# Kernel optimization log

Hardware: AMD Instinct MI355X
Metric: run time of the kernel (lower is better)

Reference implementation:

```python
import jax, jax.numpy as jnp
import numpy as np
from jax import lax


def bilinear_resize(x, oh, ow):
    # x: (..., H, W); torch F.interpolate bilinear, align_corners=False
    H, W = x.shape[-2], x.shape[-1]
    def coords(n_in, n_out):
        src = (jnp.arange(n_out, dtype=jnp.float32) + 0.5) * (n_in / n_out) - 0.5
        src = jnp.clip(src, 0.0, n_in - 1.0)
        i0 = jnp.floor(src).astype(jnp.int32)
        i1 = jnp.minimum(i0 + 1, n_in - 1)
        return i0, i1, src - i0.astype(jnp.float32)
    r0, r1, wr = coords(H, oh)
    c0, c1, wc = coords(W, ow)
    xr = x[..., r0, :] * (1.0 - wr)[:, None] + x[..., r1, :] * wr[:, None]
    return xr[..., c0] * (1.0 - wc) + xr[..., c1] * wc


def setup_inputs():
    key = jax.random.key(0)
    ks = jax.random.split(key, 20)
    B, D, C, WIN, NH, A = 256, 1280, 64, 14, 8, 49
    def p(k, *sh):
        return jax.random.normal(k, sh, dtype=jnp.float32) * 0.02
    return {
        "X": jax.random.normal(ks[0], (B, 3, D), dtype=jnp.float32),
        "W_embed": p(ks[1], C * WIN * WIN, D), "b_embed": p(ks[2], C * WIN * WIN),
        "W_qkv": p(ks[3], 3 * C, C),
        "W_proj": p(ks[4], C, C), "b_proj": p(ks[5], C),
        "dwc_w": p(ks[6], C, 1, 3, 3), "dwc_b": p(ks[7], C),
        "an_bias": p(ks[8], NH, A, 7, 7), "na_bias": p(ks[9], NH, A, 7, 7),
        "ah_bias": p(ks[10], 1, NH, A, WIN, 1), "aw_bias": p(ks[11], 1, NH, A, 1, WIN),
        "ha_bias": p(ks[12], 1, NH, WIN, 1, A), "wa_bias": p(ks[13], 1, NH, 1, WIN, A),
        "W_adj": p(ks[14], 256, C * WIN * WIN), "b_adj": p(ks[15], 256),
        "W_t1": p(ks[16], 256, D), "b_t1": p(ks[17], 256),
        "W_t2": p(ks[18], 128, 256), "b_t2": p(ks[19], 128),
    }


def reference(X, W_embed, b_embed, W_qkv, W_proj, b_proj, dwc_w, dwc_b,
              an_bias, na_bias, ah_bias, aw_bias, ha_bias, wa_bias,
              W_adj, b_adj, W_t1, b_t1, W_t2, b_t2):
    B = X.shape[0]
    C, WIN, NH, A = 64, 14, 8, 49
    N = WIN * WIN            # 196 tokens
    HD = C // NH             # head dim 8
    scale = HD ** -0.5
    b3 = 3 * B

    # embed_to_img: (B*3, 1280) -> (B*3, C*N) -> tokens (B*3, N, C)
    Xe = X.reshape(b3, -1) @ W_embed.T + b_embed
    xt = Xe.reshape(b3, N, C)

    # AgentAttention
    qkv = xt @ W_qkv.T                                  # (b3, N, 3C), qkv_bias=False
    q, k, v = jnp.split(qkv, 3, axis=-1)
    # agent tokens: AdaptiveAvgPool2d 14x14 -> 7x7 over q (exact 2x2 mean)
    agent = q.reshape(b3, 7, 2, 7, 2, C).mean(axis=(2, 4)).reshape(b3, A, C)
    q = q.reshape(b3, N, NH, HD).transpose(0, 2, 1, 3)
    k = k.reshape(b3, N, NH, HD).transpose(0, 2, 1, 3)
    v = v.reshape(b3, N, NH, HD).transpose(0, 2, 1, 3)
    agent = agent.reshape(b3, A, NH, HD).transpose(0, 2, 1, 3)

    # stage 1: agents attend to all tokens
    pb = bilinear_resize(an_bias, WIN, WIN).reshape(NH, A, N) \
         + (ah_bias + aw_bias).reshape(NH, A, N)
    agent_attn = jax.nn.softmax(jnp.einsum('bhad,bhnd->bhan', agent * scale, k) + pb, axis=-1)
    agent_v = jnp.einsum('bhan,bhnd->bhad', agent_attn, v)   # (b3, NH, A, HD)

    # stage 2: tokens attend to agents
    ab = bilinear_resize(na_bias, WIN, WIN).reshape(NH, A, N).transpose(0, 2, 1) \
         + (ha_bias + wa_bias).reshape(NH, N, A)
    q_attn = jax.nn.softmax(jnp.einsum('bhnd,bhad->bhna', q * scale, agent) + ab, axis=-1)
    o = jnp.einsum('bhna,bhad->bhnd', q_attn, agent_v)
    o = o.transpose(0, 2, 1, 3).reshape(b3, N, C)

    # depthwise conv enhancement on v
    v_img = v.transpose(0, 2, 1, 3).reshape(b3, WIN, WIN, C).transpose(0, 3, 1, 2)
    dwc = lax.conv_general_dilated(v_img, dwc_w, (1, 1), [(1, 1), (1, 1)],
                                   feature_group_count=C) + dwc_b[None, :, None, None]
    o = o + dwc.transpose(0, 2, 3, 1).reshape(b3, N, C)
    o = o @ W_proj.T + b_proj

    X_adj = (o.reshape(b3, -1) @ W_adj.T + b_adj).reshape(B, 3, -1)

    def mlp(z):
        return jnp.tanh(z @ W_t1.T + b_t1) @ W_t2.T + b_t2
    anchor, pos, neg = mlp(X[:, 0]), mlp(X[:, 1]), mlp(X[:, 2])
    return anchor, pos, neg, X_adj
```

## Files before the change

kernel.cpp:

```cpp
#include <hip/hip_runtime.h>

using u16 = unsigned short;
using u32 = unsigned int;

constexpr int Bn   = 256;
constexpr int Dd   = 1280;
constexpr int Cc   = 64;
constexpr int WINc = 14;
constexpr int NHc  = 8;
constexpr int Ac   = 49;
constexpr int Nc   = WINc * WINc;
constexpr int HDc  = Cc / NHc;
constexpr int B3c  = 3 * Bn;
constexpr int CNc  = Cc * Nc;

typedef __attribute__((ext_vector_type(8))) short v8s;
typedef __attribute__((ext_vector_type(4))) float v4f;
typedef __attribute__((ext_vector_type(2))) float v2f;

__device__ __forceinline__ float bflo(u32 u){ union{u32 x; float f;} c; c.x = u << 16; return c.f; }
__device__ __forceinline__ float bfhi(u32 u){ union{u32 x; float f;} c; c.x = u & 0xffff0000u; return c.f; }
__device__ __forceinline__ float bfs(u16 h){ union{u32 x; float f;} c; c.x = ((u32)h) << 16; return c.f; }
__device__ __forceinline__ u16 f2bb(float f){
  u32 u = __float_as_uint(f);
  u32 r = (u + 0x7fffu + ((u >> 16) & 1u)) >> 16;
  return (u16)r;
}
__device__ __forceinline__ void unpack8(uint4 u, float* dst){
  dst[0]=bflo(u.x); dst[1]=bfhi(u.x); dst[2]=bflo(u.y); dst[3]=bfhi(u.y);
  dst[4]=bflo(u.z); dst[5]=bfhi(u.z); dst[6]=bflo(u.w); dst[7]=bfhi(u.w);
}
__device__ __forceinline__ uint4 pack8(const float* s){
  uint4 r;
  r.x = (u32)f2bb(s[0]) | ((u32)f2bb(s[1]) << 16);
  r.y = (u32)f2bb(s[2]) | ((u32)f2bb(s[3]) << 16);
  r.z = (u32)f2bb(s[4]) | ((u32)f2bb(s[5]) << 16);
  r.w = (u32)f2bb(s[6]) | ((u32)f2bb(s[7]) << 16);
  return r;
}

__device__ __forceinline__ float hexp2(float x){ return __builtin_amdgcn_exp2f(x); }

__device__ __forceinline__ void gl_lds16(const u16* g, u16* l){
  __builtin_amdgcn_global_load_lds(
      (const __attribute__((address_space(1))) unsigned int*)g,
      (__attribute__((address_space(3))) unsigned int*)l,
      16, 0, 0);
}

constexpr int WeN   = 12544 * 1280;
constexpr int XN    = 768 * 1280;
constexpr int WadjN = 256 * CNc;
constexpr int W1N   = 256 * 1280;
constexpr int W2N   = 128 * 256;
constexpr int CONVB = (WeN + XN + WadjN + W1N + W2N) / (256*8);
constexpr int BIASB = (2 * NHc * Ac * Nc + 255) / 256;
__global__ __launch_bounds__(256) void conv_bias_kernel(const float* __restrict__ We,
                                                        const float* __restrict__ X,
                                                        const float* __restrict__ Wadj,
                                                        const float* __restrict__ W1,
                                                        const float* __restrict__ W2,
                                                        u16* __restrict__ WeB,
                                                        u16* __restrict__ XB,
                                                        u16* __restrict__ WadjB,
                                                        u16* __restrict__ W1B,
                                                        u16* __restrict__ W2B,
                                                        const float* __restrict__ an, const float* __restrict__ na,
                                                        const float* __restrict__ ah, const float* __restrict__ aw,
                                                        const float* __restrict__ ha, const float* __restrict__ wa,
                                                        float* __restrict__ pb, float* __restrict__ ab)
{
  if (blockIdx.x >= CONVB) {
    constexpr float LOG2E = 1.4426950408889634f;
    const int total = NHc * Ac * Nc;
    int idx = (blockIdx.x - CONVB) * 256 + threadIdx.x;
    if (idx >= 2 * total) return;
    const bool isab = idx >= total;
    const int r = isab ? idx - total : idx;
    const int h = r / (Ac * Nc);
    const int r2 = r % (Ac * Nc);
    int a, n;
    if (isab) { n = r2 / Ac; a = r2 % Ac; } else { a = r2 / Nc; n = r2 % Nc; }
    const int y = n / WINc, x = n % WINc;
    float sy = fminf(fmaxf(0.5f * y - 0.25f, 0.f), 6.f);
    float sx = fminf(fmaxf(0.5f * x - 0.25f, 0.f), 6.f);
    const int y0 = (int)sy, x0 = (int)sx;
    const float wy = sy - y0, wx = sx - x0;
    const int y1 = (y0 + 1 < 6) ? y0 + 1 : 6;
    const int x1 = (x0 + 1 < 6) ? x0 + 1 : 6;
    const float* src = (isab ? na : an) + (h * Ac + a) * 49;
    const float v00 = src[y0*7 + x0], v01 = src[y0*7 + x1];
    const float v10 = src[y1*7 + x0], v11 = src[y1*7 + x1];
    const float bi = (1.f - wy) * ((1.f - wx) * v00 + wx * v01)
                   + wy * ((1.f - wx) * v10 + wx * v11);
    if (!isab) pb[((size_t)h*Nc + n)*Ac + a] = (bi + ah[(h*Ac + a)*WINc + y] + aw[(h*Ac + a)*WINc + x]) * LOG2E;
    else       ab[((size_t)h*Ac + a)*Nc + n] = (bi + ha[(h*WINc + y)*Ac + a] + wa[(h*WINc + x)*Ac + a]) * LOG2E;
    return;
  }
  const size_t idx = ((size_t)blockIdx.x * 256 + threadIdx.x) * 8;
  const float* src; u16* dst;
  if (idx < (size_t)WeN)                          { src = We + idx;                         dst = WeB + idx; }
  else if (idx < (size_t)WeN + XN)                { src = X + (idx - WeN);                  dst = XB + (idx - WeN); }
  else if (idx < (size_t)WeN + XN + WadjN)        { src = Wadj + (idx - WeN - XN);          dst = WadjB + (idx - WeN - XN); }
  else if (idx < (size_t)WeN + XN + WadjN + W1N)  { src = W1 + (idx - WeN - XN - WadjN);    dst = W1B + (idx - WeN - XN - WadjN); }
  else                                            { src = W2 + (idx - WeN - XN - WadjN - W1N); dst = W2B + (idx - WeN - XN - WadjN - W1N); }
  float v[8];
  *reinterpret_cast<float4*>(&v[0]) = *reinterpret_cast<const float4*>(src);
  *reinterpret_cast<float4*>(&v[4]) = *reinterpret_cast<const float4*>(src + 4);
  *reinterpret_cast<uint4*>(dst) = pack8(v);
}

__global__ __launch_bounds__(256) void gemm_embed_mlp1(const u16* __restrict__ XB,
                                                       const u16* __restrict__ WeB,
                                                       const u16* __restrict__ W1B,
                                                       const float* __restrict__ be,
                                                       const float* __restrict__ b1,
                                                       u16* __restrict__ xt,
                                                       u16* __restrict__ H)
{
  constexpr int KK = Dd;
  __shared__ u16 As[128 * 32];
  __shared__ u16 Bs[128 * 32];
  const int t = threadIdx.x;
  const bool mlp = blockIdx.x >= 98;
  const int n0 = (mlp ? (blockIdx.x - 98) : blockIdx.x) * 128;
  const int m0 = blockIdx.y * 128;
  const u16* Bmat = mlp ? W1B : WeB;
  const float* bias = mlp ? b1 : be;
  u16* Cmat = mlp ? H : xt;
  const int NN = mlp ? 256 : CNc;
  const int wave = t >> 6, lane = t & 63;
  const int wm = wave >> 1, wn = wave & 1;
  const int mi = lane & 15, quad = lane >> 4;

  v4f acc[4][4];
  #pragma unroll
  for (int a = 0; a < 4; ++a)
    #pragma unroll
    for (int b = 0; b < 4; ++b) acc[a][b] = (v4f){0.f, 0.f, 0.f, 0.f};

  const int rs = wave*32 + (lane >> 2);
  const int cs = (lane & 3) * 8;
  const u16* ga0 = XB + (size_t)(m0 + rs) * KK + cs;
  const u16* ga1 = XB + (size_t)(m0 + rs + 16) * KK + cs;
  const u16* gb0 = Bmat + (size_t)(n0 + rs) * KK + cs;
  const u16* gb1 = Bmat + (size_t)(n0 + rs + 16) * KK + cs;
  u16* la0 = &As[(wave*32)      * 32];
  u16* la1 = &As[(wave*32 + 16) * 32];
  u16* lb0 = &Bs[(wave*32)      * 32];
  u16* lb1 = &Bs[(wave*32 + 16) * 32];

  for (int kt = 0; kt < KK; kt += 32) {
    gl_lds16(ga0 + kt, la0);
    gl_lds16(ga1 + kt, la1);
    gl_lds16(gb0 + kt, lb0);
    gl_lds16(gb1 + kt, lb1);
    __syncthreads();

    v8s af[4], bf[4];
    #pragma unroll
    for (int mt = 0; mt < 4; ++mt)
      af[mt] = *reinterpret_cast<const v8s*>(&As[(wm*64 + mt*16 + mi)*32 + quad*8]);
    #pragma unroll
    for (int nt = 0; nt < 4; ++nt)
      bf[nt] = *reinterpret_cast<const v8s*>(&Bs[(wn*64 + nt*16 + mi)*32 + quad*8]);
    #pragma unroll
    for (int mt = 0; mt < 4; ++mt)
      #pragma unroll
      for (int nt = 0; nt < 4; ++nt)
        acc[mt][nt] = __builtin_amdgcn_mfma_f32_16x16x32_bf16(af[mt], bf[nt], acc[mt][nt], 0, 0, 0);
    __syncthreads();
  }

  #pragma unroll
  for (int nt = 0; nt < 4; ++nt) {
    const int col = n0 + wn*64 + nt*16 + mi;
    const float bc = bias[col];
    #pragma unroll
    for (int mt = 0; mt < 4; ++mt) {
      #pragma unroll
      for (int r = 0; r < 4; ++r) {
        const int row = m0 + wm*64 + mt*16 + quad*4 + r;
        float val = acc[mt][nt][r] + bc;
        if (mlp) val = tanhf(val);
        Cmat[(size_t)row * NN + col] = f2bb(val);
      }
    }
  }
}

__global__ __launch_bounds__(256) void tail_kernel(const float* __restrict__ part,
                                                   const float* __restrict__ badj,
                                                   float* __restrict__ outadj,
                                                   const u16* __restrict__ H,
                                                   const u16* __restrict__ W2B,
                                                   const float* __restrict__ b2,
                                                   float* __restrict__ outp)
{
  __shared__ u16 As[128 * 40];
  __shared__ u16 Bs[128 * 40];
  const int t = threadIdx.x;
  if (blockIdx.x < B3c) {
    const int idx = blockIdx.x * 256 + t;
    const int n = idx & 255;
    float acc = badj[n];
    #pragma unroll
    for (int s = 0; s < 8; ++s) acc += part[(size_t)s * B3c * 256 + idx];
    outadj[idx] = acc;
    return;
  }
  const int m0 = (blockIdx.x - B3c) * 128;
  const int wave = t >> 6, lane = t & 63;
  const int wm = wave >> 1, wn = wave & 1;
  const int mi = lane & 15, quad = lane >> 4;
  const int srow = t >> 1, scol = (t & 1) * 16;

  v4f acc[4][4];
  #pragma unroll
  for (int a = 0; a < 4; ++a)
    #pragma unroll
    for (int b = 0; b < 4; ++b) acc[a][b] = (v4f){0.f, 0.f, 0.f, 0.f};

  for (int kt = 0; kt < 256; kt += 32) {
    const u16* ap = H + (size_t)(m0 + srow) * 256 + kt + scol;
    *reinterpret_cast<uint4*>(&As[srow*40 + scol])     = *reinterpret_cast<const uint4*>(ap);
    *reinterpret_cast<uint4*>(&As[srow*40 + scol + 8]) = *reinterpret_cast<const uint4*>(ap + 8);
    const u16* bp = W2B + (size_t)srow * 256 + kt + scol;
    *reinterpret_cast<uint4*>(&Bs[srow*40 + scol])     = *reinterpret_cast<const uint4*>(bp);
    *reinterpret_cast<uint4*>(&Bs[srow*40 + scol + 8]) = *reinterpret_cast<const uint4*>(bp + 8);
    __syncthreads();

    v8s af[4], bf[4];
    #pragma unroll
    for (int mt = 0; mt < 4; ++mt)
      af[mt] = *reinterpret_cast<const v8s*>(&As[(wm*64 + mt*16 + mi)*40 + quad*8]);
    #pragma unroll
    for (int nt = 0; nt < 4; ++nt)
      bf[nt] = *reinterpret_cast<const v8s*>(&Bs[(wn*64 + nt*16 + mi)*40 + quad*8]);
    #pragma unroll
    for (int mt = 0; mt < 4; ++mt)
      #pragma unroll
      for (int nt = 0; nt < 4; ++nt)
        acc[mt][nt] = __builtin_amdgcn_mfma_f32_16x16x32_bf16(af[mt], bf[nt], acc[mt][nt], 0, 0, 0);
    __syncthreads();
  }

  #pragma unroll
  for (int nt = 0; nt < 4; ++nt) {
    const int col = wn*64 + nt*16 + mi;
    const float bc = b2[col];
    #pragma unroll
    for (int mt = 0; mt < 4; ++mt) {
      #pragma unroll
      for (int r = 0; r < 4; ++r) {
        const int row = m0 + wm*64 + mt*16 + quad*4 + r;
        const int bi = row / 3, s = row - bi * 3;
        outp[(size_t)s * (Bn*128) + (size_t)bi * 128 + col] = acc[mt][nt][r] + bc;
      }
    }
  }
}

__global__ __launch_bounds__(256) void qkv_mfma(const u16* __restrict__ xt, const float* __restrict__ Wqkv,
                                                u16* __restrict__ qh, u16* __restrict__ kh, u16* __restrict__ vb)
{
  __shared__ u16 As[256 * 72];
  __shared__ u16 Bs[64 * 72];
  const int t = threadIdx.x;
  const int m0 = blockIdx.x * 256;
  const int wave = t >> 6, lane = t & 63;
  const int mi = lane & 15, quad = lane >> 4;

  {
    const int ar = t >> 2, ac = (t & 3) * 16;
    #pragma unroll
    for (int rb = 0; rb < 4; ++rb) {
      const int row = rb*64 + ar;
      const uint4* src = reinterpret_cast<const uint4*>(xt + ((size_t)(m0 + row))*64 + ac);
      *reinterpret_cast<uint4*>(&As[row*72 + ac])     = src[0];
      *reinterpret_cast<uint4*>(&As[row*72 + ac + 8]) = src[1];
    }
  }
  __syncthreads();

  v8s af[2][4];
  #pragma unroll
  for (int ks = 0; ks < 2; ++ks)
    #pragma unroll
    for (int mt = 0; mt < 4; ++mt)
      af[ks][mt] = *reinterpret_cast<const v8s*>(&As[(wave*64 + mt*16 + mi)*72 + ks*32 + quad*8]);

  #pragma unroll 1
  for (int seg = 0; seg < 3; ++seg) {
    if (seg) __syncthreads();
    for (int i = t; i < Cc*Cc; i += 256) {
      const int j = i >> 6, c = i & 63;
      Bs[j*72 + c] = f2bb(Wqkv[(size_t)(seg*64 + j)*64 + c]);
    }
    __syncthreads();

    v4f acc[4][4];
    #pragma unroll
    for (int a = 0; a < 4; ++a)
      #pragma unroll
      for (int b = 0; b < 4; ++b) acc[a][b] = (v4f){0.f, 0.f, 0.f, 0.f};

    #pragma unroll
    for (int ks = 0; ks < 2; ++ks) {
      v8s bf[4];
      #pragma unroll
      for (int nt = 0; nt < 4; ++nt)
        bf[nt] = *reinterpret_cast<const v8s*>(&Bs[(nt*16 + mi)*72 + ks*32 + quad*8]);
      #pragma unroll
      for (int mt = 0; mt < 4; ++mt)
        #pragma unroll
        for (int nt = 0; nt < 4; ++nt)
          acc[mt][nt] = __builtin_amdgcn_mfma_f32_16x16x32_bf16(af[ks][mt], bf[nt], acc[mt][nt], 0, 0, 0);
    }

    u16* hm = (seg == 0) ? qh : kh;
    #pragma unroll
    for (int nt = 0; nt < 4; ++nt) {
      const int col = nt*16 + mi;
      const int h = col >> 3, d = col & 7;
      #pragma unroll
      for (int mt = 0; mt < 4; ++mt) {
        #pragma unroll
        for (int r = 0; r < 4; ++r) {
          const int row = m0 + wave*64 + mt*16 + quad*4 + r;
          const u16 val = f2bb(acc[mt][nt][r]);
          if (seg < 2) {
            const int b = row / Nc, n = row - b * Nc;
            hm[((size_t)(b*NHc + h)*Nc + n)*8 + d] = val;
          } else {
            vb[(size_t)row * 64 + col] = val;
          }
        }
      }
    }
  }
}

__global__ __launch_bounds__(256) void attn_kernel(const u16* __restrict__ qh, const u16* __restrict__ kh,
                                                   const u16* __restrict__ v,
                                                   const float* __restrict__ pb, const float* __restrict__ ab,
                                                   u16* __restrict__ o)
{
  __shared__ float sU[Nc*10];
  __shared__ float sK[Nc*8], sV[Nc*8];
  __shared__ float sAg[Ac*8], sAV[Ac*8];
  const int bhid = blockIdx.x;
  const int h = bhid / B3c, b = bhid - h * B3c;
  const int bh = b * NHc + h;
  const int t = threadIdx.x;
  const float scale2 = 0.3535533905932738f * 1.4426950408889634f;

  float qreg[8];
  if (t < Nc) {
    const size_t base = ((size_t)bh * Nc + t) * 8;
    unpack8(*reinterpret_cast<const uint4*>(qh + base), qreg);
    #pragma unroll
    for (int d = 0; d < 8; ++d) sU[t*8 + d] = qreg[d];
    unpack8(*reinterpret_cast<const uint4*>(kh + base), &sK[t*8]);
    unpack8(*reinterpret_cast<const uint4*>(v + ((size_t)b*Nc + t)*64 + h*8), &sV[t*8]);
  }
  __syncthreads();

  for (int i = t; i < Ac*8; i += 256) {
    const int a = i >> 3, d = i & 7;
    const int ay = a / 7, ax = a % 7;
    const int n00 = (ay * 2) * WINc + ax * 2;
    sAg[i] = 0.25f * (sU[n00*8+d] + sU[(n00+1)*8+d] + sU[(n00+WINc)*8+d] + sU[(n00+WINc+1)*8+d]);
  }
  __syncthreads();

  if (t < Nc) {
    const int qd = t / Ac, a = t - qd * Ac;
    const int nb = qd * Ac;
    v2f g2[4];
    #pragma unroll
    for (int d2 = 0; d2 < 4; ++d2) g2[d2] = *reinterpret_cast<const v2f*>(&sAg[a*8 + d2*2]);
    const float* pbr = pb + ((size_t)h*Nc + nb)*Ac + a;
    float l0 = 0.f, l1 = 0.f;
    v2f avA[4] = {}, avB[4] = {};
    for (int j = 0; j < 48; j += 2) {
      const v2f* k0 = reinterpret_cast<const v2f*>(&sK[(nb + j)*8]);
      const v2f* k1 = reinterpret_cast<const v2f*>(&sK[(nb + j + 1)*8]);
      v2f sa = (g2[0]*k0[0] + g2[1]*k0[1]) + (g2[2]*k0[2] + g2[3]*k0[3]);
      v2f sb = (g2[0]*k1[0] + g2[1]*k1[1]) + (g2[2]*k1[2] + g2[3]*k1[3]);
      const float e0 = hexp2(fmaf(sa.x + sa.y, scale2, pbr[j*Ac]));
      const float e1 = hexp2(fmaf(sb.x + sb.y, scale2, pbr[(j+1)*Ac]));
      l0 += e0; l1 += e1;
      const v2f* v0 = reinterpret_cast<const v2f*>(&sV[(nb + j)*8]);
      const v2f* v1 = reinterpret_cast<const v2f*>(&sV[(nb + j + 1)*8]);
      const v2f e02 = {e0, e0}, e12 = {e1, e1};
      #pragma unroll
      for (int d2 = 0; d2 < 4; ++d2) { avA[d2] += e02 * v0[d2]; avB[d2] += e12 * v1[d2]; }
    }
    {
      const v2f* k0 = reinterpret_cast<const v2f*>(&sK[(nb + 48)*8]);
      v2f sa = (g2[0]*k0[0] + g2[1]*k0[1]) + (g2[2]*k0[2] + g2[3]*k0[3]);
      const float e0 = hexp2(fmaf(sa.x + sa.y, scale2, pbr[48*Ac]));
      l0 += e0;
      const v2f* v0 = reinterpret_cast<const v2f*>(&sV[(nb + 48)*8]);
      const v2f e02 = {e0, e0};
      #pragma unroll
      for (int d2 = 0; d2 < 4; ++d2) avA[d2] += e02 * v0[d2];
    }
    float* pp = &sU[t*9];
    pp[0] = l0 + l1;
    #pragma unroll
    for (int d2 = 0; d2 < 4; ++d2) {
      const v2f m = avA[d2] + avB[d2];
      pp[1+d2*2] = m.x; pp[2+d2*2] = m.y;
    }
  }
  __syncthreads();

  if (t < Ac) {
    float L = 0.f, av[8] = {};
    #pragma unroll
    for (int p = 0; p < 4; ++p) {
      const float* pp = &sU[(p*Ac + t)*9];
      L += pp[0];
      #pragma unroll
      for (int d = 0; d < 8; ++d) av[d] += pp[1+d];
    }
    const float inv = 1.f / L;
    #pragma unroll
    for (int d = 0; d < 8; ++d) sAV[t*8 + d] = av[d] * inv;
  }
  __syncthreads();

  if (t < Nc) {
    v2f q2[4];
    #pragma unroll
    for (int d2 = 0; d2 < 4; ++d2) q2[d2] = (v2f){qreg[d2*2], qreg[d2*2+1]};
    const float* abr = ab + (size_t)h*Ac*Nc + t;
    float l0 = 0.f, l1 = 0.f;
    v2f oA[4] = {}, oB[4] = {};
    for (int a = 0; a < 48; a += 2) {
      const v2f* g0 = reinterpret_cast<const v2f*>(&sAg[a*8]);
      const v2f* g1 = reinterpret_cast<const v2f*>(&sAg[(a+1)*8]);
      v2f sa = (q2[0]*g0[0] + q2[1]*g0[1]) + (q2[2]*g0[2] + q2[3]*g0[3]);
      v2f sb = (q2[0]*g1[0] + q2[1]*g1[1]) + (q2[2]*g1[2] + q2[3]*g1[3]);
      const float e0 = hexp2(fmaf(sa.x + sa.y, scale2, abr[a*Nc]));
      const float e1 = hexp2(fmaf(sb.x + sb.y, scale2, abr[(a+1)*Nc]));
      l0 += e0; l1 += e1;
      const v2f* a0 = reinterpret_cast<const v2f*>(&sAV[a*8]);
      const v2f* a1 = reinterpret_cast<const v2f*>(&sAV[(a+1)*8]);
      const v2f e02 = {e0, e0}, e12 = {e1, e1};
      #pragma unroll
      for (int d2 = 0; d2 < 4; ++d2) { oA[d2] += e02 * a0[d2]; oB[d2] += e12 * a1[d2]; }
    }
    {
      const v2f* g0 = reinterpret_cast<const v2f*>(&sAg[48*8]);
      v2f sa = (q2[0]*g0[0] + q2[1]*g0[1]) + (q2[2]*g0[2] + q2[3]*g0[3]);
      const float e0 = hexp2(fmaf(sa.x + sa.y, scale2, abr[48*Nc]));
      l0 += e0;
      const v2f* a0 = reinterpret_cast<const v2f*>(&sAV[48*8]);
      const v2f e02 = {e0, e0};
      #pragma unroll
      for (int d2 = 0; d2 < 4; ++d2) oA[d2] += e02 * a0[d2];
    }
    const float inv = 1.f / (l0 + l1);
    float o8[8];
    #pragma unroll
    for (int d2 = 0; d2 < 4; ++d2) {
      const v2f m = oA[d2] + oB[d2];
      o8[d2*2] = m.x * inv; o8[d2*2+1] = m.y * inv;
    }
    *reinterpret_cast<uint4*>(&o[((size_t)b*Nc + t)*64 + h*8]) = pack8(o8);
  }
}

__global__ __launch_bounds__(256) void dwc_kernel(const u16* __restrict__ o, const u16* __restrict__ v,
                                                  const float* __restrict__ dwc_w, const float* __restrict__ dwc_b,
                                                  u16* __restrict__ U)
{
  __shared__ u16 sV[Nc*Cc];
  __shared__ float sWw[9*64];
  const int b = blockIdx.x, t = threadIdx.x;

  const uint2* vsrc = reinterpret_cast<const uint2*>(v + (size_t)b * CNc);
  uint2* sV2 = reinterpret_cast<uint2*>(sV);
  for (int i = t; i < CNc/4; i += 256) sV2[i] = vsrc[i];
  for (int i = t; i < 9*64; i += 256) {
    const int k = i >> 6, c = i & 63;
    sWw[i] = dwc_w[c*9 + k];
  }
  __syncthreads();

  const int c0 = (t & 7) * 8;
  float wreg[9][8], breg[8];
  #pragma unroll
  for (int k = 0; k < 9; ++k) {
    *reinterpret_cast<float4*>(&wreg[k][0]) = *reinterpret_cast<const float4*>(&sWw[k*64 + c0]);
    *reinterpret_cast<float4*>(&wreg[k][4]) = *reinterpret_cast<const float4*>(&sWw[k*64 + c0 + 4]);
  }
  *reinterpret_cast<float4*>(&breg[0]) = *reinterpret_cast<const float4*>(dwc_b + c0);
  *reinterpret_cast<float4*>(&breg[4]) = *reinterpret_cast<const float4*>(dwc_b + c0 + 4);

  const u16* ob = o + (size_t)b * CNc;
  u16* ub = U + (size_t)b * CNc;
  for (int i = t; i < CNc/8; i += 256) {
    const int n = i >> 3;
    const int y = n / WINc, x = n % WINc;
    float acc[8], vv[8];
    unpack8(*reinterpret_cast<const uint4*>(ob + (size_t)i*8), acc);
    #pragma unroll
    for (int j = 0; j < 8; ++j) acc[j] += breg[j];
    #pragma unroll
    for (int ky = 0; ky < 3; ++ky) {
      const int yy = y + ky - 1;
      if (yy < 0 || yy >= WINc) continue;
      #pragma unroll
      for (int kx = 0; kx < 3; ++kx) {
        const int xx = x + kx - 1;
        if (xx < 0 || xx >= WINc) continue;
        const int k = ky*3 + kx;
        unpack8(*reinterpret_cast<const uint4*>(&sV[(yy*WINc + xx)*Cc + c0]), vv);
        #pragma unroll
        for (int j = 0; j < 8; ++j) acc[j] = fmaf(wreg[k][j], vv[j], acc[j]);
      }
    }
    *reinterpret_cast<uint4*>(ub + (size_t)i*8) = pack8(acc);
  }
}

__global__ __launch_bounds__(256) void proj_mfma(const u16* __restrict__ U,
                                                 const float* __restrict__ Wp,
                                                 const float* __restrict__ bp,
                                                 u16* __restrict__ oproj)
{
  __shared__ u16 As[256 * 72];
  __shared__ u16 Bs[64 * 72];
  const int t = threadIdx.x;
  const int m0 = blockIdx.x * 256;
  const int wave = t >> 6, lane = t & 63;
  const int mi = lane & 15, quad = lane >> 4;

  for (int i = t; i < Cc*Cc; i += 256) {
    const int j = i >> 6, c = i & 63;
    Bs[j*72 + c] = f2bb(Wp[i]);
  }
  {
    const int ar = t >> 2, ac = (t & 3) * 16;
    #pragma unroll
    for (int rb = 0; rb < 4; ++rb) {
      const int row = rb*64 + ar;
      const uint4* src = reinterpret_cast<const uint4*>(U + ((size_t)(m0 + row))*64 + ac);
      *reinterpret_cast<uint4*>(&As[row*72 + ac])     = src[0];
      *reinterpret_cast<uint4*>(&As[row*72 + ac + 8]) = src[1];
    }
  }
  __syncthreads();

  v4f acc[4][4];
  #pragma unroll
  for (int a = 0; a < 4; ++a)
    #pragma unroll
    for (int b = 0; b < 4; ++b) acc[a][b] = (v4f){0.f, 0.f, 0.f, 0.f};

  #pragma unroll
  for (int ks = 0; ks < 2; ++ks) {
    v8s af[4], bf[4];
    #pragma unroll
    for (int mt = 0; mt < 4; ++mt)
      af[mt] = *reinterpret_cast<const v8s*>(&As[(wave*64 + mt*16 + mi)*72 + ks*32 + quad*8]);
    #pragma unroll
    for (int nt = 0; nt < 4; ++nt)
      bf[nt] = *reinterpret_cast<const v8s*>(&Bs[(nt*16 + mi)*72 + ks*32 + quad*8]);
    #pragma unroll
    for (int mt = 0; mt < 4; ++mt)
      #pragma unroll
      for (int nt = 0; nt < 4; ++nt)
        acc[mt][nt] = __builtin_amdgcn_mfma_f32_16x16x32_bf16(af[mt], bf[nt], acc[mt][nt], 0, 0, 0);
  }

  #pragma unroll
  for (int nt = 0; nt < 4; ++nt) {
    const int col = nt*16 + mi;
    const float bc = bp[col];
    #pragma unroll
    for (int mt = 0; mt < 4; ++mt) {
      #pragma unroll
      for (int r = 0; r < 4; ++r) {
        const int row = m0 + wave*64 + mt*16 + quad*4 + r;
        oproj[(size_t)row * 64 + col] = f2bb(acc[mt][nt][r] + bc);
      }
    }
  }
}

__global__ __launch_bounds__(256) void gemm_adj_mfma(const u16* __restrict__ Amat,
                                                     const u16* __restrict__ BmatB,
                                                     float* __restrict__ part)
{
  constexpr int K = CNc, Kc = CNc/8;
  __shared__ u16 As[128 * 32];
  __shared__ u16 Bs[128 * 32];
  const int t = threadIdx.x;
  const int n0 = blockIdx.x * 128, m0 = blockIdx.y * 128;
  const int kbeg = blockIdx.z * Kc;
  const int wave = t >> 6, lane = t & 63;
  const int wm = wave >> 1, wn = wave & 1;
  const int mi = lane & 15, quad = lane >> 4;

  v4f acc[4][4];
  #pragma unroll
  for (int a = 0; a < 4; ++a)
    #pragma unroll
    for (int b = 0; b < 4; ++b) acc[a][b] = (v4f){0.f, 0.f, 0.f, 0.f};

  const int rs = wave*32 + (lane >> 2);
  const int cs = (lane & 3) * 8;
  const u16* ga0 = Amat + (size_t)(m0 + rs) * K + kbeg + cs;
  const u16* ga1 = Amat + (size_t)(m0 + rs + 16) * K + kbeg + cs;
  const u16* gb0 = BmatB + (size_t)(n0 + rs) * K + kbeg + cs;
  const u16* gb1 = BmatB + (size_t)(n0 + rs + 16) * K + kbeg + cs;
  u16* la0 = &As[(wave*32)      * 32];
  u16* la1 = &As[(wave*32 + 16) * 32];
  u16* lb0 = &Bs[(wave*32)      * 32];
  u16* lb1 = &Bs[(wave*32 + 16) * 32];

  for (int kt = 0; kt < Kc; kt += 32) {
    gl_lds16(ga0 + kt, la0);
    gl_lds16(ga1 + kt, la1);
    gl_lds16(gb0 + kt, lb0);
    gl_lds16(gb1 + kt, lb1);
    __syncthreads();

    v8s af[4], bf[4];
    #pragma unroll
    for (int mt = 0; mt < 4; ++mt)
      af[mt] = *reinterpret_cast<const v8s*>(&As[(wm*64 + mt*16 + mi)*32 + quad*8]);
    #pragma unroll
    for (int nt = 0; nt < 4; ++nt)
      bf[nt] = *reinterpret_cast<const v8s*>(&Bs[(wn*64 + nt*16 + mi)*32 + quad*8]);
    #pragma unroll
    for (int mt = 0; mt < 4; ++mt)
      #pragma unroll
      for (int nt = 0; nt < 4; ++nt)
        acc[mt][nt] = __builtin_amdgcn_mfma_f32_16x16x32_bf16(af[mt], bf[nt], acc[mt][nt], 0, 0, 0);
    __syncthreads();
  }

  const size_t zoff = (size_t)blockIdx.z * B3c * 256;
  #pragma unroll
  for (int nt = 0; nt < 4; ++nt) {
    const int col = n0 + wn*64 + nt*16 + mi;
    #pragma unroll
    for (int mt = 0; mt < 4; ++mt) {
      #pragma unroll
      for (int r = 0; r < 4; ++r) {
        const int row = m0 + wm*64 + mt*16 + quad*4 + r;
        part[zoff + (size_t)row * 256 + col] = acc[mt][nt][r];
      }
    }
  }
}

extern "C" void kernel_launch(void* const* d_in, const int* in_sizes, int n_in,
                              void* d_out, int out_size, void* d_ws, size_t ws_size,
                              hipStream_t stream)
{
  auto in = [&](int i){ return reinterpret_cast<const float*>(d_in[i]); };
  const float *X = in(0), *We = in(1), *be = in(2), *Wq = in(3), *Wp = in(4), *bp = in(5),
              *dww = in(6), *dwb = in(7), *anb = in(8), *nab = in(9), *ahb = in(10), *awb = in(11),
              *hab = in(12), *wab = in(13), *Wadj = in(14), *badj = in(15),
              *W1 = in(16), *b1 = in(17), *W2 = in(18), *b2 = in(19);
  float* out = reinterpret_cast<float*>(d_out);
  char* w = reinterpret_cast<char*>(d_ws);

  const size_t TOK = (size_t)B3c * CNc;
  u16* xt = reinterpret_cast<u16*>(w);
  u16* qh = reinterpret_cast<u16*>(w + TOK*2);
  u16* kh = reinterpret_cast<u16*>(w + TOK*4);
  u16* vb = reinterpret_cast<u16*>(w + TOK*6);
  float* pb = reinterpret_cast<float*>(w + TOK*8);
  float* ab = pb + NHc*Ac*Nc;
  u16* WadjB = reinterpret_cast<u16*>(ab + NHc*Ac*Nc);
  u16* XB  = WadjB + WadjN;
  u16* W1B = XB + XN;
  u16* W2B = W1B + W1N;
  u16* H   = W2B + W2N;
  u16* WeB = qh;
  u16* U = qh;
  float* part = reinterpret_cast<float*>(kh);

  conv_bias_kernel<<<dim3(CONVB + BIASB), 256, 0, stream>>>(
      We, X, Wadj, W1, W2, WeB, XB, WadjB, W1B, W2B,
      anb, nab, ahb, awb, hab, wab, pb, ab);
  gemm_embed_mlp1<<<dim3(100, B3c/128), 256, 0, stream>>>(XB, WeB, W1B, be, b1, xt, H);
  qkv_mfma<<<dim3((B3c*Nc)/256), 256, 0, stream>>>(xt, Wq, qh, kh, vb);
  attn_kernel<<<dim3(B3c*NHc), 256, 0, stream>>>(qh, kh, vb, pb, ab, xt );
  dwc_kernel<<<dim3(B3c), 256, 0, stream>>>(xt , vb, dww, dwb, U);
  proj_mfma<<<dim3((B3c*Nc)/256), 256, 0, stream>>>(U, Wp, bp, xt );
  gemm_adj_mfma<<<dim3(256/128, B3c/128, 8), 256, 0, stream>>>(xt , WadjB, part);
  tail_kernel<<<dim3(B3c + B3c/128), 256, 0, stream>>>(part, badj, out + 3*Bn*128, H, W2B, b2, out);
}
```

Measured before the change: 416.1 us.

## Fuse depthwise conv with output projection GEMM in one kernel

The depthwise-conv output for each sample now goes into shared memory instead of a global U buffer. The same block then runs the 64x64 projection MFMA on it and writes the result straight out. The projection weight is converted to bf16 once in the conversion kernel and kept in registers as MFMA B fragments. This removes one kernel launch and a full global write and read of the intermediate token tensor. In exchange, shared memory per block grows to roughly 55KB, which may lower occupancy, and padded rows past 196 are computed but never stored.

```diff
diff --git a/kernel.cpp b/kernel.cpp
--- a/kernel.cpp
+++ b/kernel.cpp
@@ -53,18 +53,21 @@
 constexpr int WadjN = 256 * CNc;
 constexpr int W1N   = 256 * 1280;
 constexpr int W2N   = 128 * 256;
-constexpr int CONVB = (WeN + XN + WadjN + W1N + W2N) / (256*8);
+constexpr int WpN   = 64 * 64;
+constexpr int CONVB = (WeN + XN + WadjN + W1N + W2N + WpN) / (256*8);
 constexpr int BIASB = (2 * NHc * Ac * Nc + 255) / 256;
 __global__ __launch_bounds__(256) void conv_bias_kernel(const float* __restrict__ We,
                                                         const float* __restrict__ X,
                                                         const float* __restrict__ Wadj,
                                                         const float* __restrict__ W1,
                                                         const float* __restrict__ W2,
+                                                        const float* __restrict__ Wp,
                                                         u16* __restrict__ WeB,
                                                         u16* __restrict__ XB,
                                                         u16* __restrict__ WadjB,
                                                         u16* __restrict__ W1B,
                                                         u16* __restrict__ W2B,
+                                                        u16* __restrict__ WpB,
                                                         const float* __restrict__ an, const float* __restrict__ na,
                                                         const float* __restrict__ ah, const float* __restrict__ aw,
                                                         const float* __restrict__ ha, const float* __restrict__ wa,
@@ -99,11 +102,13 @@
   }
   const size_t idx = ((size_t)blockIdx.x * 256 + threadIdx.x) * 8;
   const float* src; u16* dst;
-  if (idx < (size_t)WeN)                          { src = We + idx;                         dst = WeB + idx; }
-  else if (idx < (size_t)WeN + XN)                { src = X + (idx - WeN);                  dst = XB + (idx - WeN); }
-  else if (idx < (size_t)WeN + XN + WadjN)        { src = Wadj + (idx - WeN - XN);          dst = WadjB + (idx - WeN - XN); }
-  else if (idx < (size_t)WeN + XN + WadjN + W1N)  { src = W1 + (idx - WeN - XN - WadjN);    dst = W1B + (idx - WeN - XN - WadjN); }
-  else                                            { src = W2 + (idx - WeN - XN - WadjN - W1N); dst = W2B + (idx - WeN - XN - WadjN - W1N); }
+  size_t off = idx;
+  if (off < (size_t)WeN)            { src = We + off;   dst = WeB + off; }
+  else if ((off -= WeN) < XN)       { src = X + off;    dst = XB + off; }
+  else if ((off -= XN) < WadjN)     { src = Wadj + off; dst = WadjB + off; }
+  else if ((off -= WadjN) < W1N)    { src = W1 + off;   dst = W1B + off; }
+  else if ((off -= W1N) < W2N)      { src = W2 + off;   dst = W2B + off; }
+  else                              { off -= W2N; src = Wp + off; dst = WpB + off; }
   float v[8];
   *reinterpret_cast<float4*>(&v[0]) = *reinterpret_cast<const float4*>(src);
   *reinterpret_cast<float4*>(&v[4]) = *reinterpret_cast<const float4*>(src + 4);
@@ -474,13 +479,17 @@
   }
 }
 
-__global__ __launch_bounds__(256) void dwc_kernel(const u16* __restrict__ o, const u16* __restrict__ v,
-                                                  const float* __restrict__ dwc_w, const float* __restrict__ dwc_b,
-                                                  u16* __restrict__ U)
+__global__ __launch_bounds__(256) void dwc_proj_kernel(const u16* __restrict__ o, const u16* __restrict__ v,
+                                                       const float* __restrict__ dwc_w, const float* __restrict__ dwc_b,
+                                                       const u16* __restrict__ WpB, const float* __restrict__ bp,
+                                                       u16* __restrict__ oproj)
 {
   __shared__ u16 sV[Nc*Cc];
   __shared__ float sWw[9*64];
+  __shared__ u16 sU[208*72];
   const int b = blockIdx.x, t = threadIdx.x;
+  const int wave = t >> 6, lane = t & 63;
+  const int mi = lane & 15, quad = lane >> 4;
 
   const uint2* vsrc = reinterpret_cast<const uint2*>(v + (size_t)b * CNc);
   uint2* sV2 = reinterpret_cast<uint2*>(sV);
@@ -501,8 +510,14 @@
   *reinterpret_cast<float4*>(&breg[0]) = *reinterpret_cast<const float4*>(dwc_b + c0);
   *reinterpret_cast<float4*>(&breg[4]) = *reinterpret_cast<const float4*>(dwc_b + c0 + 4);
 
+  v8s bfr[2][4];
+  #pragma unroll
+  for (int ks = 0; ks < 2; ++ks)
+    #pragma unroll
+    for (int nt = 0; nt < 4; ++nt)
+      bfr[ks][nt] = *reinterpret_cast<const v8s*>(WpB + (size_t)(nt*16 + mi)*64 + ks*32 + quad*8);
+
   const u16* ob = o + (size_t)b * CNc;
-  u16* ub = U + (size_t)b * CNc;
   for (int i = t; i < CNc/8; i += 256) {
     const int n = i >> 3;
     const int y = n / WINc, x = n % WINc;
@@ -524,70 +539,31 @@
         for (int j = 0; j < 8; ++j) acc[j] = fmaf(wreg[k][j], vv[j], acc[j]);
       }
     }
-    *reinterpret_cast<uint4*>(ub + (size_t)i*8) = pack8(acc);
-  }
-}
-
-__global__ __launch_bounds__(256) void proj_mfma(const u16* __restrict__ U,
-                                                 const float* __restrict__ Wp,
-                                                 const float* __restrict__ bp,
-                                                 u16* __restrict__ oproj)
-{
-  __shared__ u16 As[256 * 72];
-  __shared__ u16 Bs[64 * 72];
-  const int t = threadIdx.x;
-  const int m0 = blockIdx.x * 256;
-  const int wave = t >> 6, lane = t & 63;
-  const int mi = lane & 15, quad = lane >> 4;
-
-  for (int i = t; i < Cc*Cc; i += 256) {
-    const int j = i >> 6, c = i & 63;
-    Bs[j*72 + c] = f2bb(Wp[i]);
-  }
-  {
-    const int ar = t >> 2, ac = (t & 3) * 16;
-    #pragma unroll
-    for (int rb = 0; rb < 4; ++rb) {
-      const int row = rb*64 + ar;
-      const uint4* src = reinterpret_cast<const uint4*>(U + ((size_t)(m0 + row))*64 + ac);
-      *reinterpret_cast<uint4*>(&As[row*72 + ac])     = src[0];
-      *reinterpret_cast<uint4*>(&As[row*72 + ac + 8]) = src[1];
-    }
+    *reinterpret_cast<uint4*>(&sU[n*72 + c0]) = pack8(acc);
   }
   __syncthreads();
 
-  v4f acc[4][4];
-  #pragma unroll
-  for (int a = 0; a < 4; ++a)
-    #pragma unroll
-    for (int b = 0; b < 4; ++b) acc[a][b] = (v4f){0.f, 0.f, 0.f, 0.f};
-
-  #pragma unroll
-  for (int ks = 0; ks < 2; ++ks) {
-    v8s af[4], bf[4];
-    #pragma unroll
-    for (int mt = 0; mt < 4; ++mt)
-      af[mt] = *reinterpret_cast<const v8s*>(&As[(wave*64 + mt*16 + mi)*72 + ks*32 + quad*8]);
-    #pragma unroll
-    for (int nt = 0; nt < 4; ++nt)
-      bf[nt] = *reinterpret_cast<const v8s*>(&Bs[(nt*16 + mi)*72 + ks*32 + quad*8]);
-    #pragma unroll
-    for (int mt = 0; mt < 4; ++mt)
+  u16* op = oproj + (size_t)b * CNc;
+  for (int mt = wave; mt < 13; mt += 4) {
+    v4f acc[4];
+    #pragma unroll
+    for (int nt = 0; nt < 4; ++nt) acc[nt] = (v4f){0.f, 0.f, 0.f, 0.f};
+    #pragma unroll
+    for (int ks = 0; ks < 2; ++ks) {
+      const v8s af = *reinterpret_cast<const v8s*>(&sU[(mt*16 + mi)*72 + ks*32 + quad*8]);
       #pragma unroll
       for (int nt = 0; nt < 4; ++nt)
-        acc[mt][nt] = __builtin_amdgcn_mfma_f32_16x16x32_bf16(af[mt], bf[nt], acc[mt][nt], 0, 0, 0);
-  }
-
-  #pragma unroll
-  for (int nt = 0; nt < 4; ++nt) {
-    const int col = nt*16 + mi;
-    const float bc = bp[col];
-    #pragma unroll
-    for (int mt = 0; mt < 4; ++mt) {
+        acc[nt] = __builtin_amdgcn_mfma_f32_16x16x32_bf16(af, bfr[ks][nt], acc[nt], 0, 0, 0);
+    }
+    #pragma unroll
+    for (int nt = 0; nt < 4; ++nt) {
+      const int col = nt*16 + mi;
+      const float bc = bp[col];
       #pragma unroll
       for (int r = 0; r < 4; ++r) {
-        const int row = m0 + wave*64 + mt*16 + quad*4 + r;
-        oproj[(size_t)row * 64 + col] = f2bb(acc[mt][nt][r] + bc);
+        const int row = mt*16 + quad*4 + r;
+        if (row < Nc)
+          op[(size_t)row * 64 + col] = f2bb(acc[nt][r] + bc);
       }
     }
   }
@@ -684,19 +660,18 @@
   u16* XB  = WadjB + WadjN;
   u16* W1B = XB + XN;
   u16* W2B = W1B + W1N;
-  u16* H   = W2B + W2N;
+  u16* WpB = W2B + W2N;
+  u16* H   = WpB + WpN;
   u16* WeB = qh;
-  u16* U = qh;
   float* part = reinterpret_cast<float*>(kh);
 
   conv_bias_kernel<<<dim3(CONVB + BIASB), 256, 0, stream>>>(
-      We, X, Wadj, W1, W2, WeB, XB, WadjB, W1B, W2B,
+      We, X, Wadj, W1, W2, Wp, WeB, XB, WadjB, W1B, W2B, WpB,
       anb, nab, ahb, awb, hab, wab, pb, ab);
   gemm_embed_mlp1<<<dim3(100, B3c/128), 256, 0, stream>>>(XB, WeB, W1B, be, b1, xt, H);
   qkv_mfma<<<dim3((B3c*Nc)/256), 256, 0, stream>>>(xt, Wq, qh, kh, vb);
   attn_kernel<<<dim3(B3c*NHc), 256, 0, stream>>>(qh, kh, vb, pb, ab, xt );
-  dwc_kernel<<<dim3(B3c), 256, 0, stream>>>(xt , vb, dww, dwb, U);
-  proj_mfma<<<dim3((B3c*Nc)/256), 256, 0, stream>>>(U, Wp, bp, xt );
+  dwc_proj_kernel<<<dim3(B3c), 256, 0, stream>>>(xt , vb, dww, dwb, WpB, bp, xt );
   gemm_adj_mfma<<<dim3(256/128, B3c/128, 8), 256, 0, stream>>>(xt , WadjB, part);
   tail_kernel<<<dim3(B3c + B3c/128), 256, 0, stream>>>(part, badj, out + 3*Bn*128, H, W2B, b2, out);
 }
```

Result: no change. 415.3 us (-0.2%).
